# Performance work log

Hardware: AMD Instinct MI355X
Metric: run time of the kernel (lower is better)

The kernel has to match this reference:

```python
import jax, jax.numpy as jnp
import numpy as np

B, S, D = 8, 4096, 1024
H, DH = 16, 64
DM = H * DH  # d_model = 1024


def setup_inputs() -> dict:
    key = jax.random.key(0)
    k0, k1, k2, k3 = jax.random.split(key, 4)
    x = jax.random.uniform(k0, (B, S, D), dtype=jnp.float32)
    # nn.Linear weights (stored here pre-transposed as [in, out]).
    Wq = jax.random.normal(k1, (D, DM), dtype=jnp.float32) * 0.02
    Wkv = jax.random.normal(k2, (D, 2 * DM), dtype=jnp.float32) * 0.02
    Wlin = jax.random.normal(k3, (DM, DM), dtype=jnp.float32) * 0.02
    blin = jnp.zeros((DM,), dtype=jnp.float32)
    return {"x": x, "Wq": Wq, "Wkv": Wkv, "Wlin": Wlin, "blin": blin}


def reference(x, Wq, Wkv, Wlin, blin):
    scale = DH ** (-0.5)
    # projections; cond_dim=None => cond = x (self attention), mask=None
    q = (x @ Wq).reshape(B, S, H, DH)          # [B,S,H,DH]
    kv = (x @ Wkv).reshape(B, S, H, 2 * DH)    # [B,S,H,2*DH]
    k, v = kv[..., :DH], kv[..., DH:]
    # dual softmax: q over feature dim (scaled), k over sequence dim
    q = jax.nn.softmax(q, axis=-1) * scale
    k = jax.nn.softmax(k, axis=1)              # seq axis in BSHD layout
    # context = k^T @ v per (batch, head): [B,H,DH,DH]
    context = jnp.einsum('bshd,bshe->bhde', k, v)
    # out = q @ context: [B,S,H,DH]
    out = jnp.einsum('bshd,bhde->bshe', q, context).reshape(B, S, DM)
    return out @ Wlin + blin
```

## Files before the change

kernel.cpp:

```cpp
#include <hip/hip_runtime.h>
#include <hip/hip_bf16.h>
#include <cstdint>

using bf16 = __hip_bfloat16;
typedef __attribute__((ext_vector_type(8))) short bf16x8;
typedef __attribute__((ext_vector_type(4))) float f32x4;

struct alignas(16) B8 { bf16 h[8]; };
struct alignas(8)  B4 { bf16 h[4]; };

__device__ __forceinline__ void gll16(const void* g, void* l) {
  __builtin_amdgcn_global_load_lds((__attribute__((address_space(1))) void*)g,
                                   (__attribute__((address_space(3))) void*)l,
                                   16, 0, 0);
}


__global__ __launch_bounds__(256) void cast_x_frag(const float* __restrict__ x,
                                                   bf16* __restrict__ xr) {
  __shared__ float tile[16][257];
  const int g = blockIdx.x;
  const int t = threadIdx.x;
  const float* src = x + (size_t)g * 16384;
  bf16* dst = xr + (size_t)g * 16384;
  for (int kp = 0; kp < 4; ++kp) {
    const int k0 = kp * 256;
    if (kp) __syncthreads();
    {
      const int r = t >> 4, cl = t & 15;
      #pragma unroll
      for (int s = 0; s < 16; ++s)
        tile[r][cl + 16 * s] = src[(size_t)r * 1024 + k0 + cl + 16 * s];
    }
    __syncthreads();
    #pragma unroll
    for (int rd = 0; rd < 2; ++rd) {
      const int c = rd * 256 + t;
      const int ql = c >> 4, r = c & 15;
      B8 o;
      #pragma unroll
      for (int jj = 0; jj < 8; ++jj) o.h[jj] = __float2bfloat16(tile[r][ql * 8 + jj]);
      *(B8*)(dst + ((size_t)(kp * 32 + ql) * 16 + r) * 8) = o;
    }
  }
}

__global__ __launch_bounds__(256) void wcast_frag(const float* __restrict__ W,
                                                  bf16* __restrict__ out,
                                                  int N, int n_glob0) {
  __shared__ float tw[256][17];
  const int k0 = blockIdx.x * 256;
  const int n0 = blockIdx.y * 16;
  const int t = threadIdx.x;
  {
    const int nn = t & 15, kk0 = t >> 4;
    #pragma unroll
    for (int s = 0; s < 16; ++s) {
      const int kk = kk0 + 16 * s;
      tw[kk][nn] = W[(size_t)(k0 + kk) * N + n0 + nn];
    }
  }
  __syncthreads();
  const int ng = (n_glob0 + n0) >> 4;
  #pragma unroll
  for (int rd = 0; rd < 2; ++rd) {
    const int c = rd * 256 + t;
    const int ql = c >> 4, r = c & 15;
    B8 o;
    #pragma unroll
    for (int jj = 0; jj < 8; ++jj) o.h[jj] = __float2bfloat16(tw[ql * 8 + jj][r]);
    *(B8*)(out + (((size_t)ng * 128 + (k0 >> 3) + ql) * 16 + r) * 8) = o;
  }
}

__global__ void tcast(const float* __restrict__ W, bf16* __restrict__ WT, int K, int N) {
  __shared__ float tile[32][33];
  int k0 = blockIdx.y * 32, n0 = blockIdx.x * 32;
  int tx = threadIdx.x, ty = threadIdx.y;
  for (int yy = ty; yy < 32; yy += 8)
    tile[yy][tx] = W[(size_t)(k0 + yy) * N + n0 + tx];
  __syncthreads();
  for (int yy = ty; yy < 32; yy += 8)
    WT[(size_t)(n0 + yy) * K + k0 + tx] = __float2bfloat16(tile[tx][yy]);
}

__device__ __forceinline__ void gemm_mainloop_256(
    const bf16* __restrict__ aop0, const bf16* __restrict__ aop1,
    const bf16* __restrict__ bop0, const bf16* __restrict__ bop1,
    bf16* ldsA, bf16* ldsB, int wd0, int wd1,
    int aoff, int boff, f32x4 (&acc)[8][4])
{
#define STAGE_A(slot, ko) do { gll16(aop0 + (ko) * 16, ldsA + (slot) * 8192 + wd0); \
                               gll16(aop1 + (ko) * 16, ldsA + (slot) * 8192 + wd1); } while (0)
#define STAGE_B(slot, ko) do { gll16(bop0 + (ko) * 16, ldsB + (slot) * 8192 + wd0); \
                               gll16(bop1 + (ko) * 16, ldsB + (slot) * 8192 + wd1); } while (0)
#define AFRAG(slot, i) (*(const bf16x8*)(ldsA + (slot) * 8192 + aoff + (i) * 512))
#define BFRAG(slot, j) (*(const bf16x8*)(ldsB + (slot) * 8192 + boff + (j) * 512))

  bf16x8 a1[4], a2[4], bb[2][4];

#define SECTION(S, CURB, NXTB, DO_PF, PFS, DO_ST, SLOT, KO)                         \
  do {                                                                              \
    asm volatile("s_waitcnt lgkmcnt(0)" ::: "memory");                              \
    __builtin_amdgcn_sched_barrier(0);                                              \
    __builtin_amdgcn_s_setprio(1);                                                  \
    _Pragma("unroll")                                                               \
    for (int i = 0; i < 4; i++) {                                                   \
      _Pragma("unroll")                                                             \
      for (int j = 0; j < 4; j++)                                                   \
        acc[i][j] = __builtin_amdgcn_mfma_f32_16x16x32_bf16(a1[i], bb[CURB][j],     \
                                                            acc[i][j], 0, 0, 0);    \
      a2[i] = AFRAG(S, i + 4);                                                      \
      if (DO_ST && i == 0) gll16(aop0 + (KO) * 16, ldsA + (SLOT) * 8192 + wd0);     \
      if (DO_ST && i == 1) gll16(aop1 + (KO) * 16, ldsA + (SLOT) * 8192 + wd1);     \
    }                                                                               \
    asm volatile("s_waitcnt lgkmcnt(0)" ::: "memory");                              \
    __builtin_amdgcn_sched_barrier(0);                                              \
    _Pragma("unroll")                                                               \
    for (int i = 0; i < 4; i++) {                                                   \
      _Pragma("unroll")                                                             \
      for (int j = 0; j < 4; j++)                                                   \
        acc[i + 4][j] = __builtin_amdgcn_mfma_f32_16x16x32_bf16(a2[i], bb[CURB][j], \
                                                                acc[i + 4][j], 0, 0, 0); \
      if (DO_PF) { bb[NXTB][i] = BFRAG(PFS, i); a1[i] = AFRAG(PFS, i); }            \
      if (DO_ST && i == 0) gll16(bop0 + (KO) * 16, ldsB + (SLOT) * 8192 + wd0);     \
      if (DO_ST && i == 1) gll16(bop1 + (KO) * 16, ldsB + (SLOT) * 8192 + wd1);     \
    }                                                                               \
    __builtin_amdgcn_s_setprio(0);                                                  \
  } while (0)

#define BOUNDARY(VMC)                                                               \
  do {                                                                              \
    asm volatile("s_waitcnt vmcnt(" #VMC ")" ::: "memory");                         \
    __builtin_amdgcn_s_barrier();                                                   \
    __builtin_amdgcn_sched_barrier(0);                                              \
  } while (0)

  STAGE_A(0, 0);  STAGE_B(0, 0);
  STAGE_A(1, 32); STAGE_B(1, 32);
  STAGE_A(2, 64); STAGE_B(2, 64);
  asm volatile("s_waitcnt vmcnt(4)" ::: "memory");
  __builtin_amdgcn_s_barrier();
  __builtin_amdgcn_sched_barrier(0);
  #pragma unroll
  for (int j = 0; j < 4; j++) bb[0][j] = BFRAG(0, j);
  #pragma unroll
  for (int i = 0; i < 4; i++) a1[i] = AFRAG(0, i);

  for (int q = 0; q < 7; ++q) {
    const int ko = q * 128;
    SECTION(0, 0, 1, true, 1, true, 3, ko + 96);
    BOUNDARY(4);
    SECTION(1, 1, 0, true, 2, true, 0, ko + 128);
    BOUNDARY(4);
    SECTION(2, 0, 1, true, 3, true, 1, ko + 160);
    BOUNDARY(4);
    SECTION(3, 1, 0, true, 0, true, 2, ko + 192);
    BOUNDARY(4);
  }
  SECTION(0, 0, 1, true, 1, true, 3, 992);
  BOUNDARY(4);
  SECTION(1, 1, 0, true, 2, false, 0, 0);
  BOUNDARY(0);
  SECTION(2, 0, 1, true, 3, false, 0, 0);
  BOUNDARY(0);
  SECTION(3, 1, 0, false, 0, false, 0, 0);

  __syncthreads();
#undef SECTION
#undef BOUNDARY
#undef STAGE_A
#undef STAGE_B
#undef AFRAG
#undef BFRAG
}

constexpr int QKV_NT = 12;

__global__ __launch_bounds__(512, 2)
void gemm_qkv(const bf16* __restrict__ A, const bf16* __restrict__ BT,
              bf16* __restrict__ Yq, float* __restrict__ ctxAcc)
{
  __shared__ __align__(16) union {
    struct { bf16 a[4 * 8192]; bf16 b[4 * 8192]; } g;
    struct { bf16 ekT[2][16384]; bf16 vT[2][16384]; } c;
  } sm;

  const int t = threadIdx.x;
  const int wave = t >> 6, lane = t & 63;
  const int lr = lane & 15, kq = lane >> 4;
  const int wm = wave >> 2, wn = wave & 3;
  const int bid = (int)blockIdx.x;
  const int swz = (bid & 7) * 192 + (bid >> 3);
  const int bm = swz / QKV_NT, bn = swz % QKV_NT;
  const int m0 = bm * 256, n0 = bn * 256;

  const bf16* aop0 = A + (size_t)((m0 >> 4) + wave) * 16384 + lane * 8;
  const bf16* aop1 = aop0 + 131072;
  const bf16* bop0 = BT + (size_t)((n0 >> 4) + wave) * 16384 + lane * 8;
  const bf16* bop1 = bop0 + 131072;
  const int wd0 = wave * 512;
  const int wd1 = 4096 + wave * 512;

  const int aoff = wm * 4096 + lane * 8;
  const int boff = wn * 2048 + lane * 8;

  const f32x4 zero = {0.f, 0.f, 0.f, 0.f};
  f32x4 acc[8][4];
  #pragma unroll
  for (int i = 0; i < 8; i++)
    #pragma unroll
    for (int j = 0; j < 4; j++) acc[i][j] = zero;

  gemm_mainloop_256(aop0, aop1, bop0, bop1, sm.g.a, sm.g.b, wd0, wd1,
                    aoff, boff, acc);

  if (bn < 4) {
    const int qb = (n0 + wn * 64) >> 3;
    const int jo = (lr >> 3) * 128;
    #pragma unroll
    for (int i = 0; i < 8; i++) {
      #pragma unroll
      for (int r = 0; r < 4; r++) {
        float m = fmaxf(fmaxf(acc[i][0][r], acc[i][1][r]),
                        fmaxf(acc[i][2][r], acc[i][3][r]));
        m = fmaxf(m, __shfl_xor(m, 1));
        m = fmaxf(m, __shfl_xor(m, 2));
        m = fmaxf(m, __shfl_xor(m, 4));
        m = fmaxf(m, __shfl_xor(m, 8));
        float ex[4]; float s = 0.f;
        #pragma unroll
        for (int j = 0; j < 4; j++) { ex[j] = __expf(acc[i][j][r] - m); s += ex[j]; }
        s += __shfl_xor(s, 1);
        s += __shfl_xor(s, 2);
        s += __shfl_xor(s, 4);
        s += __shfl_xor(s, 8);
        const float inv = 0.125f / s;
        const int row = m0 + wm * 128 + i * 16 + kq * 4 + r;
        bf16* yb = Yq + (((size_t)(row >> 4) * 128 + qb) * 16 + (row & 15)) * 8 + (lr & 7);
        #pragma unroll
        for (int j = 0; j < 4; j++)
          yb[j * 256 + jo] = __float2bfloat16(ex[j] * inv);
      }
    }
  } else {
    const int bb2 = m0 >> 12;
    const int h0 = (n0 - 1024) >> 7;
    const int hloc = wn >> 1, isV = wn & 1;
    bf16* const dstT = (isV ? sm.c.vT[hloc] : sm.c.ekT[hloc]);

    float zp[4] = {0.f, 0.f, 0.f, 0.f};
    #pragma unroll
    for (int i = 0; i < 8; i++) {
      const int sbase = wm * 128 + i * 16 + kq * 4;
      const int sxo = sbase >> 3;
      const int sby = (sbase & 7) * 2;
      #pragma unroll
      for (int j = 0; j < 4; j++) {
        const int d = j * 16 + lr;
        B4 pk;
        if (!isV) {
          #pragma unroll
          for (int r = 0; r < 4; r++) {
            float e = __expf(acc[i][j][r]);
            zp[j] += e;
            pk.h[r] = __float2bfloat16(e);
          }
        } else {
          #pragma unroll
          for (int r = 0; r < 4; r++) pk.h[r] = __float2bfloat16(acc[i][j][r]);
        }
        *(B4*)((char*)dstT + d * 512 + ((sxo ^ (d & 7)) << 4) + sby) = pk;
      }
    }

    if (!isV) {
      #pragma unroll
      for (int j = 0; j < 4; j++) {
        zp[j] += __shfl_xor(zp[j], 16);
        zp[j] += __shfl_xor(zp[j], 32);
      }
      if (kq == 0) {
        float* zb = ctxAcc + (size_t)(bb2 * 16 + h0 + hloc) * 4160 + 4096;
        #pragma unroll
        for (int j = 0; j < 4; j++) atomicAdd(zb + j * 16 + lr, zp[j]);
      }
    }
    __syncthreads();

    const int hh = wave >> 2, dq = wave & 3;
    const bf16* const ek = sm.c.ekT[hh];
    const bf16* const vv = sm.c.vT[hh];
    f32x4 racc[4] = {zero, zero, zero, zero};
    #pragma unroll
    for (int ks = 0; ks < 8; ks++) {
      const int ch = ks * 4 + kq;
      bf16x8 af = *(const bf16x8*)((const char*)ek + (dq * 16 + lr) * 512 + ((ch ^ (lr & 7)) << 4));
      #pragma unroll
      for (int j = 0; j < 4; j++) {
        bf16x8 bfr = *(const bf16x8*)((const char*)vv + (j * 16 + lr) * 512 + ((ch ^ (lr & 7)) << 4));
        racc[j] = __builtin_amdgcn_mfma_f32_16x16x32_bf16(af, bfr, racc[j], 0, 0, 0);
      }
    }
    float* cb = ctxAcc + (size_t)(bb2 * 16 + h0 + hh) * 4160;
    #pragma unroll
    for (int j = 0; j < 4; j++) {
      #pragma unroll
      for (int r = 0; r < 4; r++)
        atomicAdd(cb + (dq * 16 + kq * 4 + r) * 64 + j * 16 + lr, racc[j][r]);
    }
  }
}

__global__ __launch_bounds__(256) void make_w2t(const float* __restrict__ ctxAcc,
                                                const bf16* __restrict__ WlinT,
                                                bf16* __restrict__ W2T) {
  const int nc = blockIdx.x;
  const int bh = blockIdx.y;
  const int b = bh >> 4, h = bh & 15;
  const int t = threadIdx.x, lane = t & 63, w = t >> 6;
  const float* src = ctxAcc + (size_t)bh * 4160;
  const float invz = 1.0f / src[4096 + lane];
  float creg[64];
  const float* crow = src + lane * 64;
  #pragma unroll
  for (int e4 = 0; e4 < 16; e4++) {
    float4 v = *(const float4*)(crow + e4 * 4);
    creg[e4 * 4 + 0] = v.x * invz; creg[e4 * 4 + 1] = v.y * invz;
    creg[e4 * 4 + 2] = v.z * invz; creg[e4 * 4 + 3] = v.w * invz;
  }
  for (int i = 0; i < 16; i++) {
    const int n = nc * 64 + w * 16 + i;
    const bf16* wrow = WlinT + (size_t)n * 1024 + h * 64;
    float acc = 0.f;
    #pragma unroll
    for (int e8 = 0; e8 < 8; e8++) {
      B8 v = *(const B8*)(wrow + e8 * 8);
      #pragma unroll
      for (int j = 0; j < 8; j++) acc += creg[e8 * 8 + j] * __bfloat162float(v.h[j]);
    }
    W2T[(size_t)b * 1048576 +
        (((size_t)(n >> 4) * 128 + h * 8 + (lane >> 3)) * 16 + (n & 15)) * 8 + (lane & 7)]
        = __float2bfloat16(acc);
  }
}

__global__ __launch_bounds__(512, 2)
void gemm_out(const bf16* __restrict__ Aall, const bf16* __restrict__ BTall,
              float* __restrict__ Call, const float* __restrict__ bias)
{
  __shared__ __align__(16) struct { bf16 a[4 * 8192]; bf16 b[4 * 8192]; } sm;
  const int t = threadIdx.x;
  const int wave = t >> 6, lane = t & 63;
  const int lr = lane & 15, kq = lane >> 4;
  const int wm = wave >> 2, wn = wave & 3;
  const int bid = (int)blockIdx.x;
  const int swz = (bid & 7) * 64 + (bid >> 3);
  const int bz = swz >> 6;
  const int r  = swz & 63;
  const int bm = r >> 2, bn = r & 3;
  const int m0 = bm * 256, n0 = bn * 256;
  const bf16* A  = Aall  + (size_t)bz * 4194304;
  const bf16* BT = BTall + (size_t)bz * 1048576;
  float* C       = Call  + (size_t)bz * 4194304;

  const bf16* aop0 = A + (size_t)((m0 >> 4) + wave) * 16384 + lane * 8;
  const bf16* aop1 = aop0 + 131072;
  const bf16* bop0 = BT + (size_t)((n0 >> 4) + wave) * 16384 + lane * 8;
  const bf16* bop1 = bop0 + 131072;
  const int wd0 = wave * 512;
  const int wd1 = 4096 + wave * 512;

  const int aoff = wm * 4096 + lane * 8;
  const int boff = wn * 2048 + lane * 8;

  const f32x4 zero = {0.f, 0.f, 0.f, 0.f};
  f32x4 acc[8][4];
  #pragma unroll
  for (int i = 0; i < 8; i++)
    #pragma unroll
    for (int j = 0; j < 4; j++) acc[i][j] = zero;

  gemm_mainloop_256(aop0, aop1, bop0, bop1, sm.a, sm.b, wd0, wd1,
                    aoff, boff, acc);

  float bv[4];
  #pragma unroll
  for (int j = 0; j < 4; j++) bv[j] = bias[n0 + wn * 64 + j * 16 + lr];
  #pragma unroll
  for (int i = 0; i < 8; i++) {
    const int row0 = m0 + wm * 128 + i * 16 + kq * 4;
    #pragma unroll
    for (int j = 0; j < 4; j++) {
      const int col = n0 + wn * 64 + j * 16 + lr;
      const float bvj = bv[j];
      #pragma unroll
      for (int r2 = 0; r2 < 4; r2++)
        C[(size_t)(row0 + r2) * 1024 + col] = acc[i][j][r2] + bvj;
    }
  }
}

extern "C" void kernel_launch(void* const* d_in, const int* in_sizes, int n_in,
                              void* d_out, int out_size, void* d_ws, size_t ws_size,
                              hipStream_t stream) {
  (void)in_sizes; (void)n_in; (void)out_size; (void)ws_size;
  const float* x    = (const float*)d_in[0];
  const float* Wq   = (const float*)d_in[1];
  const float* Wkv  = (const float*)d_in[2];
  const float* Wlin = (const float*)d_in[3];
  const float* blin = (const float*)d_in[4];
  float* out = (float*)d_out;

  bf16* x_bf  = (bf16*)d_ws;
  bf16* WTc   = x_bf + 33554432;
  bf16* WlinT = WTc + 3145728;
  bf16* Yq    = WlinT + 1048576;
  bf16* W2T   = Yq + 33554432;
  float* ctxAcc = (float*)(W2T + 8388608);

  cast_x_frag<<<2048, 256, 0, stream>>>(x, x_bf);
  wcast_frag<<<dim3(4, 64), 256, 0, stream>>>(Wq, WTc, 1024, 0);
  wcast_frag<<<dim3(4, 128), 256, 0, stream>>>(Wkv, WTc, 2048, 1024);
  tcast<<<dim3(32, 32), dim3(32, 8), 0, stream>>>(Wlin, WlinT, 1024, 1024);

  hipMemsetAsync(ctxAcc, 0, (size_t)128 * 4160 * sizeof(float), stream);

  gemm_qkv<<<dim3(128 * QKV_NT), 512, 0, stream>>>(x_bf, WTc, Yq, ctxAcc);
  make_w2t<<<dim3(16, 128), 256, 0, stream>>>(ctxAcc, WlinT, W2T);
  gemm_out<<<dim3(512), 512, 0, stream>>>(Yq, W2T, out, blin);
}
```

Before: 370.5 us.

## Switch GEMMs from 16x16x32 to 32x32x16 MFMA with matching fragment layout

After: 416.6 us. 12.5% more time.

```diff
diff --git a/kernel.cpp b/kernel.cpp
--- a/kernel.cpp
+++ b/kernel.cpp
@@ -4,7 +4,7 @@
 
 using bf16 = __hip_bfloat16;
 typedef __attribute__((ext_vector_type(8))) short bf16x8;
-typedef __attribute__((ext_vector_type(4))) float f32x4;
+typedef __attribute__((ext_vector_type(16))) float f32x16;
 
 struct alignas(16) B8 { bf16 h[8]; };
 struct alignas(8)  B4 { bf16 h[4]; };
@@ -18,29 +18,33 @@
 
 __global__ __launch_bounds__(256) void cast_x_frag(const float* __restrict__ x,
                                                    bf16* __restrict__ xr) {
-  __shared__ float tile[16][257];
+  __shared__ float tile[32][257];
   const int g = blockIdx.x;
   const int t = threadIdx.x;
-  const float* src = x + (size_t)g * 16384;
-  bf16* dst = xr + (size_t)g * 16384;
+  const float* src = x + (size_t)g * 32768;
+  bf16* dst = xr + (size_t)g * 32768;
   for (int kp = 0; kp < 4; ++kp) {
     const int k0 = kp * 256;
     if (kp) __syncthreads();
     {
       const int r = t >> 4, cl = t & 15;
       #pragma unroll
-      for (int s = 0; s < 16; ++s)
-        tile[r][cl + 16 * s] = src[(size_t)r * 1024 + k0 + cl + 16 * s];
+      for (int hh = 0; hh < 2; ++hh)
+        #pragma unroll
+        for (int s = 0; s < 16; ++s)
+          tile[hh * 16 + r][cl + 16 * s] =
+              src[(size_t)(hh * 16 + r) * 1024 + k0 + cl + 16 * s];
     }
     __syncthreads();
     #pragma unroll
-    for (int rd = 0; rd < 2; ++rd) {
+    for (int rd = 0; rd < 4; ++rd) {
       const int c = rd * 256 + t;
-      const int ql = c >> 4, r = c & 15;
+      const int row = c & 31, sh = (c >> 5) & 1, kb = c >> 6;
       B8 o;
       #pragma unroll
-      for (int jj = 0; jj < 8; ++jj) o.h[jj] = __float2bfloat16(tile[r][ql * 8 + jj]);
-      *(B8*)(dst + ((size_t)(kp * 32 + ql) * 16 + r) * 8) = o;
+      for (int jj = 0; jj < 8; ++jj)
+        o.h[jj] = __float2bfloat16(tile[row][kb * 16 + sh * 8 + jj]);
+      *(B8*)(dst + ((size_t)kp * 1024 + c) * 8) = o;
     }
   }
 }
@@ -48,28 +52,27 @@
 __global__ __launch_bounds__(256) void wcast_frag(const float* __restrict__ W,
                                                   bf16* __restrict__ out,
                                                   int N, int n_glob0) {
-  __shared__ float tw[256][17];
+  __shared__ float tw[256][33];
   const int k0 = blockIdx.x * 256;
-  const int n0 = blockIdx.y * 16;
+  const int n0 = blockIdx.y * 32;
   const int t = threadIdx.x;
   {
-    const int nn = t & 15, kk0 = t >> 4;
-    #pragma unroll
-    for (int s = 0; s < 16; ++s) {
-      const int kk = kk0 + 16 * s;
-      tw[kk][nn] = W[(size_t)(k0 + kk) * N + n0 + nn];
-    }
+    const int nn = t & 31, kk = t >> 5;
+    #pragma unroll
+    for (int s = 0; s < 32; ++s)
+      tw[kk + 8 * s][nn] = W[(size_t)(k0 + kk + 8 * s) * N + n0 + nn];
   }
   __syncthreads();
-  const int ng = (n_glob0 + n0) >> 4;
-  #pragma unroll
-  for (int rd = 0; rd < 2; ++rd) {
+  const size_t ng = (size_t)((n_glob0 + n0) >> 5);
+  #pragma unroll
+  for (int rd = 0; rd < 4; ++rd) {
     const int c = rd * 256 + t;
-    const int ql = c >> 4, r = c & 15;
+    const int nn = c & 31, sh = (c >> 5) & 1, kb = c >> 6;
     B8 o;
     #pragma unroll
-    for (int jj = 0; jj < 8; ++jj) o.h[jj] = __float2bfloat16(tw[ql * 8 + jj][r]);
-    *(B8*)(out + (((size_t)ng * 128 + (k0 >> 3) + ql) * 16 + r) * 8) = o;
+    for (int jj = 0; jj < 8; ++jj)
+      o.h[jj] = __float2bfloat16(tw[kb * 16 + sh * 8 + jj][nn]);
+    *(B8*)(out + ((ng * 64 + (k0 >> 4) + kb) * 64 + sh * 32 + nn) * 8) = o;
   }
 }
 
@@ -85,46 +88,47 @@
 }
 
 __device__ __forceinline__ void gemm_mainloop_256(
-    const bf16* __restrict__ aop0, const bf16* __restrict__ aop1,
-    const bf16* __restrict__ bop0, const bf16* __restrict__ bop1,
-    bf16* ldsA, bf16* ldsB, int wd0, int wd1,
-    int aoff, int boff, f32x4 (&acc)[8][4])
+    const bf16* __restrict__ aop, const bf16* __restrict__ bop,
+    bf16* ldsA, bf16* ldsB, int wd, int aoff, int boff, f32x16 (&acc)[4][2])
 {
-#define STAGE_A(slot, ko) do { gll16(aop0 + (ko) * 16, ldsA + (slot) * 8192 + wd0); \
-                               gll16(aop1 + (ko) * 16, ldsA + (slot) * 8192 + wd1); } while (0)
-#define STAGE_B(slot, ko) do { gll16(bop0 + (ko) * 16, ldsB + (slot) * 8192 + wd0); \
-                               gll16(bop1 + (ko) * 16, ldsB + (slot) * 8192 + wd1); } while (0)
-#define AFRAG(slot, i) (*(const bf16x8*)(ldsA + (slot) * 8192 + aoff + (i) * 512))
-#define BFRAG(slot, j) (*(const bf16x8*)(ldsB + (slot) * 8192 + boff + (j) * 512))
-
-  bf16x8 a1[4], a2[4], bb[2][4];
-
-#define SECTION(S, CURB, NXTB, DO_PF, PFS, DO_ST, SLOT, KO)                         \
+#define SFULL(slot, ko) do { \
+    gll16(aop + (ko) * 32,       ldsA + (slot) * 8192 + wd); \
+    gll16(aop + (ko) * 32 + 512, ldsA + (slot) * 8192 + wd + 512); \
+    gll16(bop + (ko) * 32,       ldsB + (slot) * 8192 + wd); \
+    gll16(bop + (ko) * 32 + 512, ldsB + (slot) * 8192 + wd + 512); } while (0)
+#define AFRAG(slot, i, kb) (*(const bf16x8*)(ldsA + (slot) * 8192 + aoff + ((i) * 2 + (kb)) * 512))
+#define BFRAG(slot, j, kb) (*(const bf16x8*)(ldsB + (slot) * 8192 + boff + ((j) * 2 + (kb)) * 512))
+
+  bf16x8 a1[4], a2[4], b1[2], b2[2];
+
+#define SECTION(S, DO_PF, PFS, DO_ST, SLOT, KO)                                     \
   do {                                                                              \
     asm volatile("s_waitcnt lgkmcnt(0)" ::: "memory");                              \
     __builtin_amdgcn_sched_barrier(0);                                              \
     __builtin_amdgcn_s_setprio(1);                                                  \
     _Pragma("unroll")                                                               \
     for (int i = 0; i < 4; i++) {                                                   \
-      _Pragma("unroll")                                                             \
-      for (int j = 0; j < 4; j++)                                                   \
-        acc[i][j] = __builtin_amdgcn_mfma_f32_16x16x32_bf16(a1[i], bb[CURB][j],     \
-                                                            acc[i][j], 0, 0, 0);    \
-      a2[i] = AFRAG(S, i + 4);                                                      \
-      if (DO_ST && i == 0) gll16(aop0 + (KO) * 16, ldsA + (SLOT) * 8192 + wd0);     \
-      if (DO_ST && i == 1) gll16(aop1 + (KO) * 16, ldsA + (SLOT) * 8192 + wd1);     \
+      acc[i][0] = __builtin_amdgcn_mfma_f32_32x32x16_bf16(a1[i], b1[0], acc[i][0], 0, 0, 0); \
+      acc[i][1] = __builtin_amdgcn_mfma_f32_32x32x16_bf16(a1[i], b1[1], acc[i][1], 0, 0, 0); \
+      a2[i] = AFRAG(S, i, 1);                                                       \
+      if (i == 0) b2[0] = BFRAG(S, 0, 1);                                           \
+      if (i == 1) b2[1] = BFRAG(S, 1, 1);                                           \
+      if (DO_ST && i == 2) gll16(aop + (KO) * 32, ldsA + (SLOT) * 8192 + wd);       \
+      if (DO_ST && i == 3) gll16(aop + (KO) * 32 + 512, ldsA + (SLOT) * 8192 + wd + 512); \
     }                                                                               \
     asm volatile("s_waitcnt lgkmcnt(0)" ::: "memory");                              \
     __builtin_amdgcn_sched_barrier(0);                                              \
     _Pragma("unroll")                                                               \
     for (int i = 0; i < 4; i++) {                                                   \
-      _Pragma("unroll")                                                             \
-      for (int j = 0; j < 4; j++)                                                   \
-        acc[i + 4][j] = __builtin_amdgcn_mfma_f32_16x16x32_bf16(a2[i], bb[CURB][j], \
-                                                                acc[i + 4][j], 0, 0, 0); \
-      if (DO_PF) { bb[NXTB][i] = BFRAG(PFS, i); a1[i] = AFRAG(PFS, i); }            \
-      if (DO_ST && i == 0) gll16(bop0 + (KO) * 16, ldsB + (SLOT) * 8192 + wd0);     \
-      if (DO_ST && i == 1) gll16(bop1 + (KO) * 16, ldsB + (SLOT) * 8192 + wd1);     \
+      acc[i][0] = __builtin_amdgcn_mfma_f32_32x32x16_bf16(a2[i], b2[0], acc[i][0], 0, 0, 0); \
+      acc[i][1] = __builtin_amdgcn_mfma_f32_32x32x16_bf16(a2[i], b2[1], acc[i][1], 0, 0, 0); \
+      if (DO_PF) {                                                                  \
+        a1[i] = AFRAG(PFS, i, 0);                                                   \
+        if (i == 0) b1[0] = BFRAG(PFS, 0, 0);                                       \
+        if (i == 1) b1[1] = BFRAG(PFS, 1, 0);                                       \
+      }                                                                             \
+      if (DO_ST && i == 2) gll16(bop + (KO) * 32, ldsB + (SLOT) * 8192 + wd);       \
+      if (DO_ST && i == 3) gll16(bop + (KO) * 32 + 512, ldsB + (SLOT) * 8192 + wd + 512); \
     }                                                                               \
     __builtin_amdgcn_s_setprio(0);                                                  \
   } while (0)
@@ -136,41 +140,37 @@
     __builtin_amdgcn_sched_barrier(0);                                              \
   } while (0)
 
-  STAGE_A(0, 0);  STAGE_B(0, 0);
-  STAGE_A(1, 32); STAGE_B(1, 32);
-  STAGE_A(2, 64); STAGE_B(2, 64);
+  SFULL(0, 0); SFULL(1, 32); SFULL(2, 64);
   asm volatile("s_waitcnt vmcnt(4)" ::: "memory");
   __builtin_amdgcn_s_barrier();
   __builtin_amdgcn_sched_barrier(0);
-  #pragma unroll
-  for (int j = 0; j < 4; j++) bb[0][j] = BFRAG(0, j);
-  #pragma unroll
-  for (int i = 0; i < 4; i++) a1[i] = AFRAG(0, i);
+  b1[0] = BFRAG(0, 0, 0); b1[1] = BFRAG(0, 1, 0);
+  #pragma unroll
+  for (int i = 0; i < 4; i++) a1[i] = AFRAG(0, i, 0);
 
   for (int q = 0; q < 7; ++q) {
     const int ko = q * 128;
-    SECTION(0, 0, 1, true, 1, true, 3, ko + 96);
+    SECTION(0, true, 1, true, 3, ko + 96);
     BOUNDARY(4);
-    SECTION(1, 1, 0, true, 2, true, 0, ko + 128);
+    SECTION(1, true, 2, true, 0, ko + 128);
     BOUNDARY(4);
-    SECTION(2, 0, 1, true, 3, true, 1, ko + 160);
+    SECTION(2, true, 3, true, 1, ko + 160);
     BOUNDARY(4);
-    SECTION(3, 1, 0, true, 0, true, 2, ko + 192);
+    SECTION(3, true, 0, true, 2, ko + 192);
     BOUNDARY(4);
   }
-  SECTION(0, 0, 1, true, 1, true, 3, 992);
+  SECTION(0, true, 1, true, 3, 992);
   BOUNDARY(4);
-  SECTION(1, 1, 0, true, 2, false, 0, 0);
+  SECTION(1, true, 2, false, 0, 0);
   BOUNDARY(0);
-  SECTION(2, 0, 1, true, 3, false, 0, 0);
+  SECTION(2, true, 3, false, 0, 0);
   BOUNDARY(0);
-  SECTION(3, 1, 0, false, 0, false, 0, 0);
+  SECTION(3, false, 0, false, 0, 0);
 
   __syncthreads();
 #undef SECTION
 #undef BOUNDARY
-#undef STAGE_A
-#undef STAGE_B
+#undef SFULL
 #undef AFRAG
 #undef BFRAG
 }
@@ -188,59 +188,59 @@
 
   const int t = threadIdx.x;
   const int wave = t >> 6, lane = t & 63;
-  const int lr = lane & 15, kq = lane >> 4;
+  const int ln = lane & 31, hi = lane >> 5;
   const int wm = wave >> 2, wn = wave & 3;
   const int bid = (int)blockIdx.x;
   const int swz = (bid & 7) * 192 + (bid >> 3);
   const int bm = swz / QKV_NT, bn = swz % QKV_NT;
   const int m0 = bm * 256, n0 = bn * 256;
 
-  const bf16* aop0 = A + (size_t)((m0 >> 4) + wave) * 16384 + lane * 8;
-  const bf16* aop1 = aop0 + 131072;
-  const bf16* bop0 = BT + (size_t)((n0 >> 4) + wave) * 16384 + lane * 8;
-  const bf16* bop1 = bop0 + 131072;
-  const int wd0 = wave * 512;
-  const int wd1 = 4096 + wave * 512;
-
+  const bf16* aop = A + (size_t)((m0 >> 5) + wave) * 32768 + lane * 8;
+  const bf16* bop = BT + (size_t)((n0 >> 5) + wave) * 32768 + lane * 8;
+  const int wd = wave * 1024;
   const int aoff = wm * 4096 + lane * 8;
   const int boff = wn * 2048 + lane * 8;
 
-  const f32x4 zero = {0.f, 0.f, 0.f, 0.f};
-  f32x4 acc[8][4];
-  #pragma unroll
-  for (int i = 0; i < 8; i++)
-    #pragma unroll
-    for (int j = 0; j < 4; j++) acc[i][j] = zero;
-
-  gemm_mainloop_256(aop0, aop1, bop0, bop1, sm.g.a, sm.g.b, wd0, wd1,
-                    aoff, boff, acc);
+  f32x16 acc[4][2];
+  #pragma unroll
+  for (int i = 0; i < 4; i++)
+    #pragma unroll
+    for (int j = 0; j < 2; j++)
+      #pragma unroll
+      for (int e = 0; e < 16; e++) acc[i][j][e] = 0.f;
+
+  gemm_mainloop_256(aop, bop, sm.g.a, sm.g.b, wd, aoff, boff, acc);
 
   if (bn < 4) {
-    const int qb = (n0 + wn * 64) >> 3;
-    const int jo = (lr >> 3) * 128;
-    #pragma unroll
-    for (int i = 0; i < 8; i++) {
-      #pragma unroll
-      for (int r = 0; r < 4; r++) {
-        float m = fmaxf(fmaxf(acc[i][0][r], acc[i][1][r]),
-                        fmaxf(acc[i][2][r], acc[i][3][r]));
+    int cp[2];
+    #pragma unroll
+    for (int j = 0; j < 2; j++) {
+      const int c = n0 + wn * 64 + j * 32 + ln;
+      cp[j] = ((c >> 4) * 64 + ((c >> 3) & 1) * 32) * 8 + (c & 7);
+    }
+    #pragma unroll
+    for (int i = 0; i < 4; i++) {
+      #pragma unroll
+      for (int rg = 0; rg < 16; ++rg) {
+        const float v0 = acc[i][0][rg], v1 = acc[i][1][rg];
+        float m = fmaxf(v0, v1);
         m = fmaxf(m, __shfl_xor(m, 1));
         m = fmaxf(m, __shfl_xor(m, 2));
         m = fmaxf(m, __shfl_xor(m, 4));
         m = fmaxf(m, __shfl_xor(m, 8));
-        float ex[4]; float s = 0.f;
-        #pragma unroll
-        for (int j = 0; j < 4; j++) { ex[j] = __expf(acc[i][j][r] - m); s += ex[j]; }
+        m = fmaxf(m, __shfl_xor(m, 16));
+        const float e0 = __expf(v0 - m), e1 = __expf(v1 - m);
+        float s = e0 + e1;
         s += __shfl_xor(s, 1);
         s += __shfl_xor(s, 2);
         s += __shfl_xor(s, 4);
         s += __shfl_xor(s, 8);
+        s += __shfl_xor(s, 16);
         const float inv = 0.125f / s;
-        const int row = m0 + wm * 128 + i * 16 + kq * 4 + r;
-        bf16* yb = Yq + (((size_t)(row >> 4) * 128 + qb) * 16 + (row & 15)) * 8 + (lr & 7);
-        #pragma unroll
-        for (int j = 0; j < 4; j++)
-          yb[j * 256 + jo] = __float2bfloat16(ex[j] * inv);
+        const int row = m0 + wm * 128 + i * 32 + (rg & 3) + 8 * (rg >> 2) + 4 * hi;
+        const size_t rp = ((size_t)(row >> 5) * 4096 + (row & 31)) * 8;
+        Yq[rp + cp[0]] = __float2bfloat16(e0 * inv);
+        Yq[rp + cp[1]] = __float2bfloat16(e1 * inv);
       }
     }
   } else {
@@ -249,65 +249,59 @@
     const int hloc = wn >> 1, isV = wn & 1;
     bf16* const dstT = (isV ? sm.c.vT[hloc] : sm.c.ekT[hloc]);
 
-    float zp[4] = {0.f, 0.f, 0.f, 0.f};
-    #pragma unroll
-    for (int i = 0; i < 8; i++) {
-      const int sbase = wm * 128 + i * 16 + kq * 4;
-      const int sxo = sbase >> 3;
-      const int sby = (sbase & 7) * 2;
-      #pragma unroll
-      for (int j = 0; j < 4; j++) {
-        const int d = j * 16 + lr;
-        B4 pk;
-        if (!isV) {
+    float zp[2] = {0.f, 0.f};
+    #pragma unroll
+    for (int i = 0; i < 4; i++) {
+      #pragma unroll
+      for (int j = 0; j < 2; j++) {
+        char* base = (char*)dstT + ((wm * 8 + i * 2) * 2 + j) * 1024 + ln * 16 + hi * 8;
+        #pragma unroll
+        for (int q = 0; q < 4; ++q) {
+          B4 pk;
           #pragma unroll
-          for (int r = 0; r < 4; r++) {
-            float e = __expf(acc[i][j][r]);
-            zp[j] += e;
-            pk.h[r] = __float2bfloat16(e);
+          for (int r = 0; r < 4; ++r) {
+            const float v = acc[i][j][q * 4 + r];
+            if (!isV) {
+              const float e = __expf(v);
+              zp[j] += e;
+              pk.h[r] = __float2bfloat16(e);
+            } else {
+              pk.h[r] = __float2bfloat16(v);
+            }
           }
-        } else {
-          #pragma unroll
-          for (int r = 0; r < 4; r++) pk.h[r] = __float2bfloat16(acc[i][j][r]);
+          *(B4*)(base + (q >> 1) * 2048 + (q & 1) * 512) = pk;
         }
-        *(B4*)((char*)dstT + d * 512 + ((sxo ^ (d & 7)) << 4) + sby) = pk;
       }
     }
 
     if (!isV) {
-      #pragma unroll
-      for (int j = 0; j < 4; j++) {
-        zp[j] += __shfl_xor(zp[j], 16);
-        zp[j] += __shfl_xor(zp[j], 32);
+      zp[0] += __shfl_xor(zp[0], 32);
+      zp[1] += __shfl_xor(zp[1], 32);
+      if (hi == 0) {
+        float* zb = ctxAcc + (size_t)(bb2 * 16 + h0 + hloc) * 4160 + 4096;
+        atomicAdd(zb + ln, zp[0]);
+        atomicAdd(zb + 32 + ln, zp[1]);
       }
-      if (kq == 0) {
-        float* zb = ctxAcc + (size_t)(bb2 * 16 + h0 + hloc) * 4160 + 4096;
-        #pragma unroll
-        for (int j = 0; j < 4; j++) atomicAdd(zb + j * 16 + lr, zp[j]);
-      }
     }
     __syncthreads();
 
-    const int hh = wave >> 2, dq = wave & 3;
-    const bf16* const ek = sm.c.ekT[hh];
-    const bf16* const vv = sm.c.vT[hh];
-    f32x4 racc[4] = {zero, zero, zero, zero};
-    #pragma unroll
-    for (int ks = 0; ks < 8; ks++) {
-      const int ch = ks * 4 + kq;
-      bf16x8 af = *(const bf16x8*)((const char*)ek + (dq * 16 + lr) * 512 + ((ch ^ (lr & 7)) << 4));
-      #pragma unroll
-      for (int j = 0; j < 4; j++) {
-        bf16x8 bfr = *(const bf16x8*)((const char*)vv + (j * 16 + lr) * 512 + ((ch ^ (lr & 7)) << 4));
-        racc[j] = __builtin_amdgcn_mfma_f32_16x16x32_bf16(af, bfr, racc[j], 0, 0, 0);
-      }
+    const int hh = wave >> 2, D = (wave >> 1) & 1, E = wave & 1;
+    const char* ek = (const char*)sm.c.ekT[hh];
+    const char* vv = (const char*)sm.c.vT[hh];
+    f32x16 racc;
+    #pragma unroll
+    for (int e = 0; e < 16; e++) racc[e] = 0.f;
+    #pragma unroll
+    for (int kb = 0; kb < 16; ++kb) {
+      bf16x8 af  = *(const bf16x8*)(ek + (kb * 2 + D) * 1024 + lane * 16);
+      bf16x8 bfr = *(const bf16x8*)(vv + (kb * 2 + E) * 1024 + lane * 16);
+      racc = __builtin_amdgcn_mfma_f32_32x32x16_bf16(af, bfr, racc, 0, 0, 0);
     }
     float* cb = ctxAcc + (size_t)(bb2 * 16 + h0 + hh) * 4160;
     #pragma unroll
-    for (int j = 0; j < 4; j++) {
-      #pragma unroll
-      for (int r = 0; r < 4; r++)
-        atomicAdd(cb + (dq * 16 + kq * 4 + r) * 64 + j * 16 + lr, racc[j][r]);
+    for (int rg = 0; rg < 16; ++rg) {
+      const int d = D * 32 + (rg & 3) + 8 * (rg >> 2) + 4 * hi;
+      atomicAdd(cb + d * 64 + E * 32 + ln, racc[rg]);
     }
   }
 }
@@ -340,8 +334,8 @@
       for (int j = 0; j < 8; j++) acc += creg[e8 * 8 + j] * __bfloat162float(v.h[j]);
     }
     W2T[(size_t)b * 1048576 +
-        (((size_t)(n >> 4) * 128 + h * 8 + (lane >> 3)) * 16 + (n & 15)) * 8 + (lane & 7)]
-        = __float2bfloat16(acc);
+        (((size_t)(n >> 5) * 64 + h * 4 + (lane >> 4)) * 64 + ((lane >> 3) & 1) * 32 + (n & 31)) * 8
+        + (lane & 7)] = __float2bfloat16(acc);
   }
 }
 
@@ -352,7 +346,7 @@
   __shared__ __align__(16) struct { bf16 a[4 * 8192]; bf16 b[4 * 8192]; } sm;
   const int t = threadIdx.x;
   const int wave = t >> 6, lane = t & 63;
-  const int lr = lane & 15, kq = lane >> 4;
+  const int ln = lane & 31, hi = lane >> 5;
   const int wm = wave >> 2, wn = wave & 3;
   const int bid = (int)blockIdx.x;
   const int swz = (bid & 7) * 64 + (bid >> 3);
@@ -364,39 +358,33 @@
   const bf16* BT = BTall + (size_t)bz * 1048576;
   float* C       = Call  + (size_t)bz * 4194304;
 
-  const bf16* aop0 = A + (size_t)((m0 >> 4) + wave) * 16384 + lane * 8;
-  const bf16* aop1 = aop0 + 131072;
-  const bf16* bop0 = BT + (size_t)((n0 >> 4) + wave) * 16384 + lane * 8;
-  const bf16* bop1 = bop0 + 131072;
-  const int wd0 = wave * 512;
-  const int wd1 = 4096 + wave * 512;
-
+  const bf16* aop = A + (size_t)((m0 >> 5) + wave) * 32768 + lane * 8;
+  const bf16* bop = BT + (size_t)((n0 >> 5) + wave) * 32768 + lane * 8;
+  const int wd = wave * 1024;
   const int aoff = wm * 4096 + lane * 8;
   const int boff = wn * 2048 + lane * 8;
 
-  const f32x4 zero = {0.f, 0.f, 0.f, 0.f};
-  f32x4 acc[8][4];
-  #pragma unroll
-  for (int i = 0; i < 8; i++)
-    #pragma unroll
-    for (int j = 0; j < 4; j++) acc[i][j] = zero;
-
-  gemm_mainloop_256(aop0, aop1, bop0, bop1, sm.a, sm.b, wd0, wd1,
-                    aoff, boff, acc);
-
-  float bv[4];
-  #pragma unroll
-  for (int j = 0; j < 4; j++) bv[j] = bias[n0 + wn * 64 + j * 16 + lr];
-  #pragma unroll
-  for (int i = 0; i < 8; i++) {
-    const int row0 = m0 + wm * 128 + i * 16 + kq * 4;
-    #pragma unroll
-    for (int j = 0; j < 4; j++) {
-      const int col = n0 + wn * 64 + j * 16 + lr;
-      const float bvj = bv[j];
-      #pragma unroll
-      for (int r2 = 0; r2 < 4; r2++)
-        C[(size_t)(row0 + r2) * 1024 + col] = acc[i][j][r2] + bvj;
+  f32x16 acc[4][2];
+  #pragma unroll
+  for (int i = 0; i < 4; i++)
+    #pragma unroll
+    for (int j = 0; j < 2; j++)
+      #pragma unroll
+      for (int e = 0; e < 16; e++) acc[i][j][e] = 0.f;
+
+  gemm_mainloop_256(aop, bop, sm.a, sm.b, wd, aoff, boff, acc);
+
+  float bv[2];
+  #pragma unroll
+  for (int j = 0; j < 2; j++) bv[j] = bias[n0 + wn * 64 + j * 32 + ln];
+  const int col0 = n0 + wn * 64 + ln;
+  #pragma unroll
+  for (int i = 0; i < 4; i++) {
+    #pragma unroll
+    for (int rg = 0; rg < 16; ++rg) {
+      const int row = m0 + wm * 128 + i * 32 + (rg & 3) + 8 * (rg >> 2) + 4 * hi;
+      C[(size_t)row * 1024 + col0]      = acc[i][0][rg] + bv[0];
+      C[(size_t)row * 1024 + col0 + 32] = acc[i][1][rg] + bv[1];
     }
   }
 }
@@ -419,9 +407,9 @@
   bf16* W2T   = Yq + 33554432;
   float* ctxAcc = (float*)(W2T + 8388608);
 
-  cast_x_frag<<<2048, 256, 0, stream>>>(x, x_bf);
-  wcast_frag<<<dim3(4, 64), 256, 0, stream>>>(Wq, WTc, 1024, 0);
-  wcast_frag<<<dim3(4, 128), 256, 0, stream>>>(Wkv, WTc, 2048, 1024);
+  cast_x_frag<<<1024, 256, 0, stream>>>(x, x_bf);
+  wcast_frag<<<dim3(4, 32), 256, 0, stream>>>(Wq, WTc, 1024, 0);
+  wcast_frag<<<dim3(4, 64), 256, 0, stream>>>(Wkv, WTc, 2048, 1024);
   tcast<<<dim3(32, 32), dim3(32, 8), 0, stream>>>(Wlin, WlinT, 1024, 1024);
 
   hipMemsetAsync(ctxAcc, 0, (size_t)128 * 4160 * sizeof(float), stream);
```
